# Performance work log

Measured on AMD Instinct MI355X. Metric: run time of the kernel, lower is better.

## Reference

```python
import jax, jax.numpy as jnp
import numpy as np

B, C, N = 16, 256, 2048  # C = channels_m, inputs have C//2 channels
C2 = C // 2
BN_EPS = 1e-5


def setup_inputs() -> dict:
    key = jax.random.key(0)
    ks = jax.random.split(key, 8)
    s = 1.0 / np.sqrt(C2)
    return {
        "q": jax.random.normal(ks[0], (B, C2, N), dtype=jnp.float32),
        "x": jax.random.normal(ks[1], (B, C2, N), dtype=jnp.float32),
        "Wq": jax.random.normal(ks[2], (C2, C2), dtype=jnp.float32) * s,
        "Wk": jax.random.normal(ks[3], (C2, C2), dtype=jnp.float32) * s,
        "Wv": jax.random.normal(ks[4], (C, C2), dtype=jnp.float32) * s,
        "bv": jax.random.normal(ks[5], (C,), dtype=jnp.float32) * 0.01,
        "Wt": jax.random.normal(ks[6], (C, C), dtype=jnp.float32) * (1.0 / np.sqrt(C)),
        "bt": jax.random.normal(ks[7], (C,), dtype=jnp.float32) * 0.01,
        "gamma": jnp.ones((C,), dtype=jnp.float32),
        "beta": jnp.zeros((C,), dtype=jnp.float32),
        "running_mean": jnp.zeros((C,), dtype=jnp.float32),
        "running_var": jnp.ones((C,), dtype=jnp.float32),
    }


def reference(q, x, Wq, Wk, Wv, bv, Wt, bt, gamma, beta, running_mean, running_var):
    # 1x1 Conv1d == channel matmul. q, x: [B, C2, N]
    x_q = jnp.einsum('oc,bcn->bno', Wq, q)                     # [B, N, C2]
    x_k = jnp.einsum('oc,bcn->bon', Wk, x)                     # [B, C2, N]
    x_v = jnp.einsum('oc,bcn->bon', Wv, q) + bv[None, :, None]  # [B, C, N]

    energy = jnp.einsum('bnc,bcm->bnm', x_q, x_k)              # [B, N, N]
    attn = jax.nn.softmax(energy, axis=-1)
    # extra column-wise L1 renormalization (offset-attention)
    attn = attn / (1e-9 + attn.sum(axis=1, keepdims=True))

    x_r = jnp.einsum('bcn,bnm->bcm', x_v, attn)                # [B, C, N]
    x2 = jnp.einsum('oc,bcn->bon', Wv, x) + bv[None, :, None]  # v_conv(x): [B, C, N]

    t = jnp.einsum('oc,bcn->bon', Wt, x2 - x_r) + bt[None, :, None]
    inv = gamma * jax.lax.rsqrt(running_var + BN_EPS)
    bn = t * inv[None, :, None] + (beta - running_mean * inv)[None, :, None]
    return jax.nn.relu(bn) + x2
```

## Files before the change

kernel.cpp:

```cpp
#include <hip/hip_runtime.h>
#include <hip/hip_bf16.h>
#include <math.h>

#define BB 16
#define CC 256
#define C2 128
#define NN 2048

typedef __attribute__((ext_vector_type(8))) _Float16 f16x8;
typedef __attribute__((ext_vector_type(8))) short bf16x8;
typedef __attribute__((ext_vector_type(16))) float f32x16;
typedef unsigned short u16;

#define OFF_X2   ((size_t)0)
#define OFF_U16  ((size_t)16777216)
#define UOFF_XQT ((size_t)0)
#define UOFF_XKT ((size_t)4194304)
#define UOFF_XV  ((size_t)8388608)
#define OFF_RMAX ((size_t)25165824)
#define OFF_RSUM ((size_t)25198592)
#define OFF_W16  ((size_t)29458432)
#define WOFF_WQ  ((size_t)0)
#define WOFF_WK  ((size_t)16384)
#define WOFF_WV  ((size_t)32768)
#define WOFF_WT  ((size_t)65536)

__device__ __forceinline__ u16 f2h(float f) {
    union { _Float16 h; u16 u; } v; v.h = (_Float16)f;
    return v.u;
}
__device__ __forceinline__ u16 f2bf(float f) {
    union { float f; unsigned u; } v; v.f = f;
    return (u16)((v.u + 0x7fffu + ((v.u >> 16) & 1u)) >> 16);
}

__global__ __launch_bounds__(256) void prep_w(
    const float* __restrict__ Wq, const float* __restrict__ Wk,
    const float* __restrict__ Wv, const float* __restrict__ Wt,
    u16* __restrict__ w16)
{
    int i = blockIdx.x * 256 + threadIdx.x;
    float v; u16* dst; int o, c, KC;
    if (i < 16384)      { v = Wq[i]; o = i >> 7; c = i & 127; KC = 16; dst = w16; }
    else if (i < 32768) { int j = i - 16384; v = Wk[j]; o = j >> 7; c = j & 127; KC = 16; dst = w16 + 16384; }
    else if (i < 65536) { int j = i - 32768; v = Wv[j]; o = j >> 7; c = j & 127; KC = 16; dst = w16 + 32768; }
    else                { int j = i - 65536; v = Wt[j]; o = j >> 8; c = j & 255; KC = 32; dst = w16 + 65536; }
    int idx = (((o >> 5) * KC + (c >> 3)) << 8) + ((o & 31) << 3) + (c & 7);
    dst[idx] = f2h(v);
}

__global__ __launch_bounds__(256, 2) void proj_fused(
    const float* __restrict__ q, const float* __restrict__ x,
    const u16* __restrict__ wq16, const u16* __restrict__ wk16,
    const u16* __restrict__ wv16, const float* __restrict__ bias,
    u16* __restrict__ xqT, u16* __restrict__ xkT,
    u16* __restrict__ xv_bf, float* __restrict__ x2_f32)
{
    __shared__ u16 t_s[64 * 136];
    __shared__ u16 st[16384];
    int tid = threadIdx.x, lane = tid & 63, wave = tid >> 6;
    int zb = blockIdx.z, b = zb >> 1, which = zb & 1;
    int n0 = blockIdx.x * 64;
    const float* in  = which ? x : q;
    const u16*   wqk = which ? wk16 : wq16;
    u16*         outT = which ? xkT : xqT;
    {
        int r = tid >> 2;
        int nc = (tid & 3) * 16;
        #pragma unroll
        for (int hh = 0; hh < 2; ++hh) {
            const float4* ip4 = (const float4*)(in + ((size_t)b * C2 + hh * 64 + r) * NN + n0 + nc);
            #pragma unroll
            for (int jj = 0; jj < 4; ++jj) {
                float4 v = ip4[jj];
                int nbase = nc + jj * 4;
                t_s[(nbase + 0) * 136 + hh * 64 + r] = f2h(v.x);
                t_s[(nbase + 1) * 136 + hh * 64 + r] = f2h(v.y);
                t_s[(nbase + 2) * 136 + hh * 64 + r] = f2h(v.z);
                t_s[(nbase + 3) * 136 + hh * 64 + r] = f2h(v.w);
            }
        }
    }
    __syncthreads();
    int nsub = wave & 1, g = wave >> 1;
    int lrow = lane & 31, h = lane >> 5, lk8 = h * 8;
    const u16* brow = &t_s[(nsub * 32 + lrow) * 136 + lk8];
    f32x16 aq0, aq1, av0, av1, av2, av3;
    #pragma unroll
    for (int r = 0; r < 16; ++r)
        { aq0[r]=0.f; aq1[r]=0.f; av0[r]=0.f; av1[r]=0.f; av2[r]=0.f; av3[r]=0.f; }
    const u16* wqA = wqk  + (size_t)(2 * g) * 4096 + h * 256 + lrow * 8;
    const u16* wvA = wv16 + (size_t)(4 * g) * 4096 + h * 256 + lrow * 8;
    #pragma unroll
    for (int kk = 0; kk < 8; ++kk) {
        f16x8 bf = *(const f16x8*)&brow[kk * 16];
        f16x8 q0 = *(const f16x8*)&wqA[kk * 512];
        f16x8 q1 = *(const f16x8*)&wqA[4096 + kk * 512];
        aq0 = __builtin_amdgcn_mfma_f32_32x32x16_f16(bf, q0, aq0, 0, 0, 0);
        aq1 = __builtin_amdgcn_mfma_f32_32x32x16_f16(bf, q1, aq1, 0, 0, 0);
        f16x8 v0 = *(const f16x8*)&wvA[kk * 512];
        f16x8 v1 = *(const f16x8*)&wvA[4096 + kk * 512];
        f16x8 v2 = *(const f16x8*)&wvA[8192 + kk * 512];
        f16x8 v3 = *(const f16x8*)&wvA[12288 + kk * 512];
        av0 = __builtin_amdgcn_mfma_f32_32x32x16_f16(v0, bf, av0, 0, 0, 0);
        av1 = __builtin_amdgcn_mfma_f32_32x32x16_f16(v1, bf, av1, 0, 0, 0);
        av2 = __builtin_amdgcn_mfma_f32_32x32x16_f16(v2, bf, av2, 0, 0, 0);
        av3 = __builtin_amdgcn_mfma_f32_32x32x16_f16(v3, bf, av3, 0, 0, 0);
    }
    __syncthreads();
    {
        int off = (nsub * 16 + g * 8 + (lrow >> 3)) * 256 + (lrow & 7);
        #pragma unroll
        for (int r = 0; r < 16; ++r) {
            int ro = (r & 3) + 8 * (r >> 2) + 4 * h;
            t_s[off + ro * 8]        = f2h(aq0[r]);
            t_s[off + 1024 + ro * 8] = f2h(aq1[r]);
        }
    }
    if (which == 0) {
        int off = (g * 4 * 8 + nsub * 4 + (lrow >> 3)) * 256 + (lrow & 7);
        #pragma unroll
        for (int r = 0; r < 16; ++r) {
            int ro = (r & 3) + 8 * (r >> 2) + 4 * h;
            int c0r = g * 128 + ro;
            st[off + ro * 8]        = f2bf(av0[r] + bias[c0r]);
            st[off + 2048 + ro * 8] = f2bf(av1[r] + bias[c0r + 32]);
            st[off + 4096 + ro * 8] = f2bf(av2[r] + bias[c0r + 64]);
            st[off + 6144 + ro * 8] = f2bf(av3[r] + bias[c0r + 96]);
        }
    }
    __syncthreads();
    {
        u16* outb = outT + (size_t)b * NN * C2 + (size_t)(n0 >> 5) * 4096;
        for (int i = tid; i < 1024; i += 256)
            *(uint4*)&outb[i * 8] = *(uint4*)&t_s[i * 8];
    }
    if (which == 0) {
        u16* xvb = xv_bf + (size_t)b * CC * NN + (size_t)(n0 >> 3) * 256;
        for (int i = tid; i < 2048; i += 256) {
            int ct = i >> 8, j = i & 255;
            *(uint4*)&xvb[(size_t)ct * 65536 + j * 8] = *(uint4*)&st[ct * 2048 + j * 8];
        }
    } else {
        int n = n0 + nsub * 32 + lrow;
        #pragma unroll
        for (int r = 0; r < 16; ++r) {
            int ro = (r & 3) + 8 * (r >> 2) + 4 * h;
            int c0r = g * 128 + ro;
            x2_f32[((size_t)b * CC + c0r) * NN + n]      = av0[r] + bias[c0r];
            x2_f32[((size_t)b * CC + c0r + 32) * NN + n] = av1[r] + bias[c0r + 32];
            x2_f32[((size_t)b * CC + c0r + 64) * NN + n] = av2[r] + bias[c0r + 64];
            x2_f32[((size_t)b * CC + c0r + 96) * NN + n] = av3[r] + bias[c0r + 96];
        }
    }
}

__global__ __launch_bounds__(512, 4) void rowstats_mfma(
    const u16* __restrict__ xqT, const u16* __restrict__ xkT,
    float* __restrict__ rmax, float* __restrict__ rsum)
{
    __shared__ float Mp[8][32];
    __shared__ float Sp[8][32];
    const int tid  = threadIdx.x;
    int flat = blockIdx.x + gridDim.x * blockIdx.y;
    int xcd = flat & 7, rank = flat >> 3;
    const int b  = xcd * 2 + (rank >> 5);
    const int n0 = (rank & 31) * 64;
    const int lane = tid & 63;
    const int wave = tid >> 6;
    const int lrow = lane & 31;
    const int h    = lane >> 5;
    const u16* xqb = xqT + (size_t)b * NN * C2;
    const u16* xkb = xkT + (size_t)b * NN * C2;
    const int mquad = wave >> 1, nsub = wave & 1;

    f16x8 bR[8];
    {
        const u16* bp = xqb + ((size_t)((n0 >> 5) + nsub) * 16) * 256 + h * 256 + lrow * 8;
        #pragma unroll
        for (int kk = 0; kk < 8; ++kk) bR[kk] = *(const f16x8*)&bp[kk * 512];
    }
    float runM = -1e30f, runS = 0.f;
    const u16* ap = xkb + (size_t)(mquad * 16) * 256 + h * 256 + lrow * 8;
    for (int m0 = 0; m0 < NN; m0 += 128) {
        f32x16 e0;
        #pragma unroll
        for (int r = 0; r < 16; ++r) e0[r] = 0.f;
        #pragma unroll
        for (int kk = 0; kk < 8; ++kk) {
            f16x8 a0 = *(const f16x8*)&ap[kk * 512];
            e0 = __builtin_amdgcn_mfma_f32_32x32x16_f16(a0, bR[kk], e0, 0, 0, 0);
        }
        ap += 16384;
        float tm = e0[0];
        #pragma unroll
        for (int r = 1; r < 16; ++r) tm = fmaxf(tm, e0[r]);
        float newM = fmaxf(runM, tm);
        float sc = __expf(runM - newM);
        float ts = 0.f;
        #pragma unroll
        for (int r = 0; r < 16; ++r) ts += __expf(e0[r] - newM);
        runS = runS * sc + ts;
        runM = newM;
    }
    float oM = __shfl_xor(runM, 32, 64);
    float oS = __shfl_xor(runS, 32, 64);
    float M2 = fmaxf(runM, oM);
    float S2 = runS * __expf(runM - M2) + oS * __expf(oM - M2);
    if (lane < 32) { Mp[wave][lane] = M2; Sp[wave][lane] = S2; }
    __syncthreads();
    if (tid < 64) {
        int ns = tid >> 5, li = tid & 31;
        float Ma = Mp[ns][li],     Mb = Mp[ns + 2][li];
        float Mc = Mp[ns + 4][li], Md = Mp[ns + 6][li];
        float Mf = fmaxf(fmaxf(Ma, Mb), fmaxf(Mc, Md));
        float Sf = Sp[ns][li]     * __expf(Ma - Mf) + Sp[ns + 2][li] * __expf(Mb - Mf)
                 + Sp[ns + 4][li] * __expf(Mc - Mf) + Sp[ns + 6][li] * __expf(Md - Mf);
        rmax[(size_t)b * NN + n0 + tid] = Mf;
        rsum[(size_t)b * NN + n0 + tid] = Sf;
    }
}

__global__ __launch_bounds__(512, 4) void pv_mfma(
    const u16* __restrict__ xqT, const u16* __restrict__ xkT,
    const u16* __restrict__ xv, const float* __restrict__ rmax,
    const float* __restrict__ rsum, const float* __restrict__ x2,
    const u16* __restrict__ wt16, const float* __restrict__ bt,
    const float* __restrict__ gamma, const float* __restrict__ beta,
    const float* __restrict__ rmean, const float* __restrict__ rvar,
    float* __restrict__ out)
{
    __shared__ __align__(16) u16 smem[19584];
    const int tid = threadIdx.x;
    int flat = blockIdx.x + gridDim.x * blockIdx.y;
    int xcd = flat & 7, rank = flat >> 3;
    const int b  = xcd * 2 + (rank >> 5);
    const int m0 = (rank & 31) * 64;
    const int lane = tid & 63;
    const int wave = tid >> 6;
    const int lrow = lane & 31;
    const int h    = lane >> 5;
    const int lk8  = h * 8;
    const u16* xqb = xqT + (size_t)b * NN * C2;
    const u16* xkb = xkT + (size_t)b * NN * C2;
    const u16* xvb = xv  + (size_t)b * CC * NN;
    const float* rmx = rmax + (size_t)b * NN;
    const float* rsm = rsum + (size_t)b * NN;

    if (tid < 256) {
        float iv = gamma[tid] * rsqrtf(rvar[tid] + 1e-5f);
        float* bn = (float*)(smem + 18560);
        bn[tid]       = iv;
        bn[256 + tid] = bt[tid] * iv + beta[tid] - rmean[tid] * iv;
    }

    f16x8 aK[8];
    {
        const u16* kp = xkb + ((size_t)((m0 >> 5) + (wave & 1)) * 16) * 256 + h * 256 + lrow * 8;
        #pragma unroll
        for (int kk = 0; kk < 8; ++kk) aK[kk] = *(const f16x8*)&kp[kk * 512];
    }
    const int nq = wave >> 1;
    const int nl = nq * 32 + lrow;
    const int mbase = (wave & 1) * 32 + 4 * h;
    const u16* bqbase = xqb + (size_t)nq * 4096 + h * 256 + lrow * 8;
    const u16* avbase = xvb + (size_t)wave * 65536 + h * 256 + lrow * 8;

    f32x16 acc00, acc01;
    #pragma unroll
    for (int r = 0; r < 16; ++r) { acc00[r] = 0.f; acc01[r] = 0.f; }
    float s_reg = 0.f;
    __syncthreads();

    for (int ph = 0; ph <= 16; ++ph) {
        f16x8 bq[8];
        float Mn = 0.f, Sn = 1.f;
        if (ph < 16) {
            const u16* bqp = bqbase + (size_t)ph * 16384;
            #pragma unroll
            for (int kk = 0; kk < 8; ++kk) bq[kk] = *(const f16x8*)&bqp[kk * 512];
            Mn = rmx[ph * 128 + nl];
            Sn = rsm[ph * 128 + nl];
        }
        if (ph >= 1) {
            const int t = ph - 1;
            const u16* p_prev = smem + (t & 1) * 8704;
            const u16* avp = avbase + (size_t)t * 4096;
            {
                const uint4* prp = (const uint4*)&p_prev[(tid & 63) * 136 + (tid >> 6) * 16];
                uint4 v0 = prp[0], v1 = prp[1];
                unsigned wsv[8] = {v0.x, v0.y, v0.z, v0.w, v1.x, v1.y, v1.z, v1.w};
                float ss = 0.f;
                #pragma unroll
                for (int j = 0; j < 8; ++j) {
                    union { unsigned u; float f; } lo, hi;
                    lo.u = wsv[j] << 16;
                    hi.u = wsv[j] & 0xffff0000u;
                    ss += lo.f + hi.f;
                }
                s_reg += ss;
            }
            const u16* br0 = &p_prev[lrow * 136 + lk8];
            const u16* br1 = &p_prev[(32 + lrow) * 136 + lk8];
            __builtin_amdgcn_s_setprio(1);
            #pragma unroll
            for (int kk = 0; kk < 8; ++kk) {
                bf16x8 a0 = *(const bf16x8*)&avp[kk * 512];
                bf16x8 b0 = *(const bf16x8*)&br0[kk * 16];
                bf16x8 b1 = *(const bf16x8*)&br1[kk * 16];
                acc00 = __builtin_amdgcn_mfma_f32_32x32x16_bf16(a0, b0, acc00, 0, 0, 0);
                acc01 = __builtin_amdgcn_mfma_f32_32x32x16_bf16(a0, b1, acc01, 0, 0, 0);
            }
            __builtin_amdgcn_s_setprio(0);
        }
        if (ph < 16) {
            f32x16 e0;
            #pragma unroll
            for (int r = 0; r < 16; ++r) e0[r] = 0.f;
            __builtin_amdgcn_s_setprio(1);
            #pragma unroll
            for (int kk = 0; kk < 8; ++kk)
                e0 = __builtin_amdgcn_mfma_f32_32x32x16_f16(aK[kk], bq[kk], e0, 0, 0, 0);
            __builtin_amdgcn_s_setprio(0);
            float Si = 1.f / Sn;
            u16* p_cur = smem + (ph & 1) * 8704;
            #pragma unroll
            for (int r = 0; r < 16; ++r) {
                int ml = mbase + (r & 3) + 8 * (r >> 2);
                p_cur[ml * 136 + nl] = f2bf(__expf(e0[r] - Mn) * Si);
            }
        }
        __syncthreads();
    }
    float* s_part = (float*)(smem + 17408);
    s_part[(tid & 63) * 8 + (tid >> 6)] = s_reg;
    __syncthreads();
    float* sinv = (float*)(smem + 18432);
    if (tid < 64) {
        float ss = 0.f;
        #pragma unroll
        for (int j = 0; j < 8; ++j) ss += s_part[tid * 8 + j];
        sinv[tid] = 1.f / (1e-9f + ss);
    }
    __syncthreads();
    u16* dts = smem;
    const float* x2b = x2 + (size_t)b * CC * NN;
    float si0 = sinv[lrow], si1 = sinv[32 + lrow];
    #pragma unroll
    for (int r = 0; r < 16; ++r) {
        int ro = (r & 3) + 8 * (r >> 2) + 4 * h;
        int c = wave * 32 + ro;
        float d0 = x2b[(size_t)c * NN + m0 + lrow]      - acc00[r] * si0;
        float d1 = x2b[(size_t)c * NN + m0 + 32 + lrow] - acc01[r] * si1;
        dts[lrow * 264 + c]        = f2h(d0);
        dts[(32 + lrow) * 264 + c] = f2h(d1);
    }
    __syncthreads();
    {
        float* inv_s = (float*)(smem + 18560);
        float* add_s = inv_s + 256;
        int rt0 = (wave >> 1) * 2;
        int ns2 = wave & 1;
        const u16* brow2 = &dts[(ns2 * 32 + lrow) * 264 + lk8];
        const u16* a0p = wt16 + (size_t)rt0 * 8192 + h * 256 + lrow * 8;
        const u16* a1p = a0p + 8192;
        f32x16 o0a, o1a;
        #pragma unroll
        for (int r = 0; r < 16; ++r) { o0a[r] = 0.f; o1a[r] = 0.f; }
        #pragma unroll
        for (int kk = 0; kk < 16; ++kk) {
            f16x8 bb2 = *(const f16x8*)&brow2[kk * 16];
            f16x8 a0 = *(const f16x8*)&a0p[kk * 512];
            f16x8 a1 = *(const f16x8*)&a1p[kk * 512];
            o0a = __builtin_amdgcn_mfma_f32_32x32x16_f16(a0, bb2, o0a, 0, 0, 0);
            o1a = __builtin_amdgcn_mfma_f32_32x32x16_f16(a1, bb2, o1a, 0, 0, 0);
        }
        int n = m0 + ns2 * 32 + lrow;
        float* outb = out + (size_t)b * CC * NN;
        #pragma unroll
        for (int r = 0; r < 16; ++r) {
            int ro = (r & 3) + 8 * (r >> 2) + 4 * h;
            int ol0 = rt0 * 32 + ro, ol1 = ol0 + 32;
            float t0 = o0a[r] * inv_s[ol0] + add_s[ol0];
            float t1 = o1a[r] * inv_s[ol1] + add_s[ol1];
            outb[(size_t)ol0 * NN + n] = fmaxf(t0, 0.f) + x2b[(size_t)ol0 * NN + n];
            outb[(size_t)ol1 * NN + n] = fmaxf(t1, 0.f) + x2b[(size_t)ol1 * NN + n];
        }
    }
}

extern "C" void kernel_launch(void* const* d_in, const int* in_sizes, int n_in,
                              void* d_out, int out_size, void* d_ws, size_t ws_size,
                              hipStream_t stream)
{
    const float* q     = (const float*)d_in[0];
    const float* x     = (const float*)d_in[1];
    const float* Wq    = (const float*)d_in[2];
    const float* Wk    = (const float*)d_in[3];
    const float* Wv    = (const float*)d_in[4];
    const float* bv    = (const float*)d_in[5];
    const float* Wt    = (const float*)d_in[6];
    const float* bt    = (const float*)d_in[7];
    const float* gamma = (const float*)d_in[8];
    const float* beta  = (const float*)d_in[9];
    const float* rmean = (const float*)d_in[10];
    const float* rvar  = (const float*)d_in[11];
    float* out = (float*)d_out;
    float* ws  = (float*)d_ws;

    float* x2   = ws + OFF_X2;
    u16*   u1   = (u16*)(ws + OFF_U16);
    u16*   xqT  = u1 + UOFF_XQT;
    u16*   xkT  = u1 + UOFF_XKT;
    u16*   xv   = u1 + UOFF_XV;
    float* rmax = ws + OFF_RMAX;
    float* rsum = ws + OFF_RSUM;
    u16*   w16  = (u16*)(ws + OFF_W16);

    dim3 blk(256);
    prep_w<<<dim3(512), blk, 0, stream>>>(Wq, Wk, Wv, Wt, w16);
    proj_fused<<<dim3(NN/64, 1, 2*BB), blk, 0, stream>>>(
        q, x, w16 + WOFF_WQ, w16 + WOFF_WK, w16 + WOFF_WV, bv,
        xqT, xkT, xv, x2);
    rowstats_mfma<<<dim3(NN/64, BB), dim3(512), 0, stream>>>(xqT, xkT, rmax, rsum);
    pv_mfma<<<dim3(NN/64, BB), dim3(512), 0, stream>>>(
        xqT, xkT, xv, rmax, rsum, x2, w16 + WOFF_WT, bt, gamma, beta,
        rmean, rvar, out);
}
```

Measured before the change: 249.7 us.

## Merge all stages into one cooperative persistent kernel with grid syncs

Replaces the four separate launches (weight prep, projection, row stats, PV+output) with one cooperative kernel. The stages are separated by grid.sync, and each block loops over work units in a grid-stride loop. The projection stage is reorganised for 512-thread blocks: each block handles both the q and x inputs for one tile, so per-wave accumulator usage is lower. The aim is to remove launch gaps and inter-kernel drain, at the cost of grid-barrier overhead and occupancy limited by the cooperative launch.

```diff
diff --git a/kernel.cpp b/kernel.cpp
--- a/kernel.cpp
+++ b/kernel.cpp
@@ -1,6 +1,9 @@
 #include <hip/hip_runtime.h>
+#include <hip/hip_cooperative_groups.h>
 #include <hip/hip_bf16.h>
 #include <math.h>
+
+namespace cg = cooperative_groups;
 
 #define BB 16
 #define CC 256
@@ -34,357 +37,362 @@
     return (u16)((v.u + 0x7fffu + ((v.u >> 16) & 1u)) >> 16);
 }
 
-__global__ __launch_bounds__(256) void prep_w(
+__global__ __launch_bounds__(512, 4) void fused_all(
+    const float* __restrict__ q, const float* __restrict__ x,
     const float* __restrict__ Wq, const float* __restrict__ Wk,
-    const float* __restrict__ Wv, const float* __restrict__ Wt,
-    u16* __restrict__ w16)
+    const float* __restrict__ Wv, const float* __restrict__ bv,
+    const float* __restrict__ Wt, const float* __restrict__ bt,
+    const float* __restrict__ gamma, const float* __restrict__ beta,
+    const float* __restrict__ rmean, const float* __restrict__ rvar,
+    float* __restrict__ out, float* __restrict__ ws)
 {
-    int i = blockIdx.x * 256 + threadIdx.x;
-    float v; u16* dst; int o, c, KC;
-    if (i < 16384)      { v = Wq[i]; o = i >> 7; c = i & 127; KC = 16; dst = w16; }
-    else if (i < 32768) { int j = i - 16384; v = Wk[j]; o = j >> 7; c = j & 127; KC = 16; dst = w16 + 16384; }
-    else if (i < 65536) { int j = i - 32768; v = Wv[j]; o = j >> 7; c = j & 127; KC = 16; dst = w16 + 32768; }
-    else                { int j = i - 65536; v = Wt[j]; o = j >> 8; c = j & 255; KC = 32; dst = w16 + 65536; }
-    int idx = (((o >> 5) * KC + (c >> 3)) << 8) + ((o & 31) << 3) + (c & 7);
-    dst[idx] = f2h(v);
-}
-
-__global__ __launch_bounds__(256, 2) void proj_fused(
-    const float* __restrict__ q, const float* __restrict__ x,
-    const u16* __restrict__ wq16, const u16* __restrict__ wk16,
-    const u16* __restrict__ wv16, const float* __restrict__ bias,
-    u16* __restrict__ xqT, u16* __restrict__ xkT,
-    u16* __restrict__ xv_bf, float* __restrict__ x2_f32)
-{
-    __shared__ u16 t_s[64 * 136];
-    __shared__ u16 st[16384];
-    int tid = threadIdx.x, lane = tid & 63, wave = tid >> 6;
-    int zb = blockIdx.z, b = zb >> 1, which = zb & 1;
-    int n0 = blockIdx.x * 64;
-    const float* in  = which ? x : q;
-    const u16*   wqk = which ? wk16 : wq16;
-    u16*         outT = which ? xkT : xqT;
-    {
-        int r = tid >> 2;
-        int nc = (tid & 3) * 16;
+    float* x2   = ws + OFF_X2;
+    u16*   u1   = (u16*)(ws + OFF_U16);
+    u16*   xqT  = u1 + UOFF_XQT;
+    u16*   xkT  = u1 + UOFF_XKT;
+    u16*   xv   = u1 + UOFF_XV;
+    float* rmax = ws + OFF_RMAX;
+    float* rsum = ws + OFF_RSUM;
+    u16*   w16  = (u16*)(ws + OFF_W16);
+
+    __shared__ __align__(16) u16 smem[19584];
+    const int tid = threadIdx.x;
+    const int nb  = gridDim.x;
+    cg::grid_group grid = cg::this_grid();
+
+    for (int i = blockIdx.x * 512 + tid; i < 131072; i += nb * 512) {
+        float v; u16* dst; int o, c, KC;
+        if (i < 16384)      { v = Wq[i]; o = i >> 7; c = i & 127; KC = 16; dst = w16; }
+        else if (i < 32768) { int j = i - 16384; v = Wk[j]; o = j >> 7; c = j & 127; KC = 16; dst = w16 + 16384; }
+        else if (i < 65536) { int j = i - 32768; v = Wv[j]; o = j >> 7; c = j & 127; KC = 16; dst = w16 + 32768; }
+        else                { int j = i - 65536; v = Wt[j]; o = j >> 8; c = j & 255; KC = 32; dst = w16 + 65536; }
+        dst[(((o >> 5) * KC + (c >> 3)) << 8) + ((o & 31) << 3) + (c & 7)] = f2h(v);
+    }
+    __threadfence();
+    grid.sync();
+
+    for (int wu = blockIdx.x; wu < 512; wu += nb) {
+        const int lane = tid & 63, wave = tid >> 6;
+        const int lrow = lane & 31, h = lane >> 5, lk8 = h * 8;
+        const int b  = wu & 15;
+        const int n0 = (wu >> 4) * 64;
+        const int nsub = wave & 1, gp = wave >> 1;
+        u16* t_s = smem;
+        u16* stg = smem + 8704;
+        const u16* wv16 = w16 + WOFF_WV;
+
         #pragma unroll
-        for (int hh = 0; hh < 2; ++hh) {
-            const float4* ip4 = (const float4*)(in + ((size_t)b * C2 + hh * 64 + r) * NN + n0 + nc);
-            #pragma unroll
-            for (int jj = 0; jj < 4; ++jj) {
-                float4 v = ip4[jj];
-                int nbase = nc + jj * 4;
-                t_s[(nbase + 0) * 136 + hh * 64 + r] = f2h(v.x);
-                t_s[(nbase + 1) * 136 + hh * 64 + r] = f2h(v.y);
-                t_s[(nbase + 2) * 136 + hh * 64 + r] = f2h(v.z);
-                t_s[(nbase + 3) * 136 + hh * 64 + r] = f2h(v.w);
+        for (int u = 0; u < 2; ++u) {
+            const float* in  = u ? x : q;
+            const u16*   wqk = u ? (w16 + WOFF_WK) : (w16 + WOFF_WQ);
+            __syncthreads();
+            {
+                int c = tid >> 2;
+                int qn = (tid & 3) * 16;
+                const float4* ip4 = (const float4*)(in + ((size_t)b * C2 + c) * NN + n0 + qn);
+                #pragma unroll
+                for (int jj = 0; jj < 4; ++jj) {
+                    float4 v = ip4[jj];
+                    int nbv = qn + jj * 4;
+                    t_s[(nbv + 0) * 136 + c] = f2h(v.x);
+                    t_s[(nbv + 1) * 136 + c] = f2h(v.y);
+                    t_s[(nbv + 2) * 136 + c] = f2h(v.z);
+                    t_s[(nbv + 3) * 136 + c] = f2h(v.w);
+                }
+            }
+            __syncthreads();
+            f32x16 aq0, av0, av1;
+            #pragma unroll
+            for (int r = 0; r < 16; ++r) { aq0[r] = 0.f; av0[r] = 0.f; av1[r] = 0.f; }
+            const u16* brow = &t_s[(nsub * 32 + lrow) * 136 + lk8];
+            const u16* wqA  = wqk  + (size_t)gp * 4096 + h * 256 + lrow * 8;
+            const u16* wvA0 = wv16 + (size_t)(gp * 2) * 4096 + h * 256 + lrow * 8;
+            const u16* wvA1 = wvA0 + 4096;
+            #pragma unroll
+            for (int kk = 0; kk < 8; ++kk) {
+                f16x8 bf = *(const f16x8*)&brow[kk * 16];
+                f16x8 q0 = *(const f16x8*)&wqA[kk * 512];
+                aq0 = __builtin_amdgcn_mfma_f32_32x32x16_f16(bf, q0, aq0, 0, 0, 0);
+                f16x8 v0 = *(const f16x8*)&wvA0[kk * 512];
+                f16x8 v1 = *(const f16x8*)&wvA1[kk * 512];
+                av0 = __builtin_amdgcn_mfma_f32_32x32x16_f16(v0, bf, av0, 0, 0, 0);
+                av1 = __builtin_amdgcn_mfma_f32_32x32x16_f16(v1, bf, av1, 0, 0, 0);
+            }
+            {
+                int off = (nsub * 16 + gp * 4 + (lrow >> 3)) * 256 + (lrow & 7);
+                #pragma unroll
+                for (int r = 0; r < 16; ++r) {
+                    int ro = (r & 3) + 8 * (r >> 2) + 4 * h;
+                    stg[off + ro * 8] = f2h(aq0[r]);
+                }
+            }
+            __syncthreads();
+            {
+                u16* outb = (u ? xkT : xqT) + (size_t)b * NN * C2 + (size_t)(n0 >> 5) * 4096;
+                for (int i = tid; i < 1024; i += 512)
+                    *(uint4*)&outb[i * 8] = *(uint4*)&stg[i * 8];
+            }
+            if (u == 0) {
+                #pragma unroll
+                for (int ct2 = 0; ct2 < 2; ++ct2) {
+                    __syncthreads();
+                    if ((gp >> 1) == ct2) {
+                        int off = (((gp & 1) * 2) * 8 + nsub * 4 + (lrow >> 3)) * 256 + (lrow & 7);
+                        #pragma unroll
+                        for (int r = 0; r < 16; ++r) {
+                            int ro = (r & 3) + 8 * (r >> 2) + 4 * h;
+                            int c0 = gp * 64 + ro;
+                            stg[off + ro * 8]        = f2bf(av0[r] + bv[c0]);
+                            stg[off + 2048 + ro * 8] = f2bf(av1[r] + bv[c0 + 32]);
+                        }
+                    }
+                    __syncthreads();
+                    u16* xvb = xv + (size_t)b * CC * NN + (size_t)(ct2 * 4) * 65536
+                                  + (size_t)(n0 >> 3) * 256;
+                    for (int i = tid; i < 1024; i += 512) {
+                        int ctile = i >> 8;
+                        int m8 = (i & 255) * 8;
+                        *(uint4*)&xvb[(size_t)ctile * 65536 + m8] =
+                            *(uint4*)&stg[ctile * 2048 + m8];
+                    }
+                }
+            } else {
+                float* x2b = x2 + (size_t)b * CC * NN;
+                int n = n0 + nsub * 32 + lrow;
+                #pragma unroll
+                for (int r = 0; r < 16; ++r) {
+                    int ro = (r & 3) + 8 * (r >> 2) + 4 * h;
+                    int c0 = gp * 64 + ro;
+                    x2b[(size_t)c0 * NN + n]        = av0[r] + bv[c0];
+                    x2b[(size_t)(c0 + 32) * NN + n] = av1[r] + bv[c0 + 32];
+                }
             }
         }
     }
-    __syncthreads();
-    int nsub = wave & 1, g = wave >> 1;
-    int lrow = lane & 31, h = lane >> 5, lk8 = h * 8;
-    const u16* brow = &t_s[(nsub * 32 + lrow) * 136 + lk8];
-    f32x16 aq0, aq1, av0, av1, av2, av3;
-    #pragma unroll
-    for (int r = 0; r < 16; ++r)
-        { aq0[r]=0.f; aq1[r]=0.f; av0[r]=0.f; av1[r]=0.f; av2[r]=0.f; av3[r]=0.f; }
-    const u16* wqA = wqk  + (size_t)(2 * g) * 4096 + h * 256 + lrow * 8;
-    const u16* wvA = wv16 + (size_t)(4 * g) * 4096 + h * 256 + lrow * 8;
-    #pragma unroll
-    for (int kk = 0; kk < 8; ++kk) {
-        f16x8 bf = *(const f16x8*)&brow[kk * 16];
-        f16x8 q0 = *(const f16x8*)&wqA[kk * 512];
-        f16x8 q1 = *(const f16x8*)&wqA[4096 + kk * 512];
-        aq0 = __builtin_amdgcn_mfma_f32_32x32x16_f16(bf, q0, aq0, 0, 0, 0);
-        aq1 = __builtin_amdgcn_mfma_f32_32x32x16_f16(bf, q1, aq1, 0, 0, 0);
-        f16x8 v0 = *(const f16x8*)&wvA[kk * 512];
-        f16x8 v1 = *(const f16x8*)&wvA[4096 + kk * 512];
-        f16x8 v2 = *(const f16x8*)&wvA[8192 + kk * 512];
-        f16x8 v3 = *(const f16x8*)&wvA[12288 + kk * 512];
-        av0 = __builtin_amdgcn_mfma_f32_32x32x16_f16(v0, bf, av0, 0, 0, 0);
-        av1 = __builtin_amdgcn_mfma_f32_32x32x16_f16(v1, bf, av1, 0, 0, 0);
-        av2 = __builtin_amdgcn_mfma_f32_32x32x16_f16(v2, bf, av2, 0, 0, 0);
-        av3 = __builtin_amdgcn_mfma_f32_32x32x16_f16(v3, bf, av3, 0, 0, 0);
+    __threadfence();
+    grid.sync();
+
+    for (int wu = blockIdx.x; wu < 512; wu += nb) {
+        __syncthreads();
+        float* Mp = (float*)smem;
+        float* Sp = Mp + 256;
+        const int lane = tid & 63;
+        const int wave = tid >> 6;
+        const int lrow = lane & 31;
+        const int h    = lane >> 5;
+        int xcd = wu & 7, rank = wu >> 3;
+        const int b  = xcd * 2 + (rank >> 5);
+        const int n0 = (rank & 31) * 64;
+        const u16* xqb = xqT + (size_t)b * NN * C2;
+        const u16* xkb = xkT + (size_t)b * NN * C2;
+        const int mquad = wave >> 1, nsub = wave & 1;
+
+        f16x8 bR[8];
+        {
+            const u16* bp = xqb + ((size_t)((n0 >> 5) + nsub) * 16) * 256 + h * 256 + lrow * 8;
+            #pragma unroll
+            for (int kk = 0; kk < 8; ++kk) bR[kk] = *(const f16x8*)&bp[kk * 512];
+        }
+        float runM = -1e30f, runS = 0.f;
+        const u16* ap = xkb + (size_t)(mquad * 16) * 256 + h * 256 + lrow * 8;
+        for (int m0 = 0; m0 < NN; m0 += 128) {
+            f32x16 e0;
+            #pragma unroll
+            for (int r = 0; r < 16; ++r) e0[r] = 0.f;
+            #pragma unroll
+            for (int kk = 0; kk < 8; ++kk) {
+                f16x8 a0 = *(const f16x8*)&ap[kk * 512];
+                e0 = __builtin_amdgcn_mfma_f32_32x32x16_f16(a0, bR[kk], e0, 0, 0, 0);
+            }
+            ap += 16384;
+            float tm = e0[0];
+            #pragma unroll
+            for (int r = 1; r < 16; ++r) tm = fmaxf(tm, e0[r]);
+            float newM = fmaxf(runM, tm);
+            float sc = __expf(runM - newM);
+            float ts = 0.f;
+            #pragma unroll
+            for (int r = 0; r < 16; ++r) ts += __expf(e0[r] - newM);
+            runS = runS * sc + ts;
+            runM = newM;
+        }
+        float oM = __shfl_xor(runM, 32, 64);
+        float oS = __shfl_xor(runS, 32, 64);
+        float M2 = fmaxf(runM, oM);
+        float S2 = runS * __expf(runM - M2) + oS * __expf(oM - M2);
+        if (lane < 32) { Mp[wave * 32 + lane] = M2; Sp[wave * 32 + lane] = S2; }
+        __syncthreads();
+        if (tid < 64) {
+            int ns = tid >> 5, li = tid & 31;
+            float Ma = Mp[ns * 32 + li],       Mb = Mp[(ns + 2) * 32 + li];
+            float Mc = Mp[(ns + 4) * 32 + li], Md = Mp[(ns + 6) * 32 + li];
+            float Mf = fmaxf(fmaxf(Ma, Mb), fmaxf(Mc, Md));
+            float Sf = Sp[ns * 32 + li]       * __expf(Ma - Mf)
+                     + Sp[(ns + 2) * 32 + li] * __expf(Mb - Mf)
+                     + Sp[(ns + 4) * 32 + li] * __expf(Mc - Mf)
+                     + Sp[(ns + 6) * 32 + li] * __expf(Md - Mf);
+            rmax[(size_t)b * NN + n0 + tid] = Mf;
+            rsum[(size_t)b * NN + n0 + tid] = Sf;
+        }
     }
-    __syncthreads();
-    {
-        int off = (nsub * 16 + g * 8 + (lrow >> 3)) * 256 + (lrow & 7);
+    __threadfence();
+    grid.sync();
+
+    for (int wu = blockIdx.x; wu < 512; wu += nb) {
+        __syncthreads();
+        const int lane = tid & 63;
+        const int wave = tid >> 6;
+        const int lrow = lane & 31;
+        const int h    = lane >> 5;
+        const int lk8  = h * 8;
+        int xcd = wu & 7, rank = wu >> 3;
+        const int b  = xcd * 2 + (rank >> 5);
+        const int m0 = (rank & 31) * 64;
+        const u16* xqb = xqT + (size_t)b * NN * C2;
+        const u16* xkb = xkT + (size_t)b * NN * C2;
+        const u16* xvb = xv  + (size_t)b * CC * NN;
+        const float* rmx = rmax + (size_t)b * NN;
+        const float* rsm = rsum + (size_t)b * NN;
+        const u16* wt16 = w16 + WOFF_WT;
+
+        if (tid < 256) {
+            float iv = gamma[tid] * rsqrtf(rvar[tid] + 1e-5f);
+            float* bn = (float*)(smem + 18560);
+            bn[tid]       = iv;
+            bn[256 + tid] = bt[tid] * iv + beta[tid] - rmean[tid] * iv;
+        }
+        f16x8 aK[8];
+        {
+            const u16* kp = xkb + ((size_t)((m0 >> 5) + (wave & 1)) * 16) * 256 + h * 256 + lrow * 8;
+            #pragma unroll
+            for (int kk = 0; kk < 8; ++kk) aK[kk] = *(const f16x8*)&kp[kk * 512];
+        }
+        const int nq = wave >> 1;
+        const int nl = nq * 32 + lrow;
+        const int mbase = (wave & 1) * 32 + 4 * h;
+        const u16* bqbase = xqb + (size_t)nq * 4096 + h * 256 + lrow * 8;
+        const u16* avbase = xvb + (size_t)wave * 65536 + h * 256 + lrow * 8;
+
+        f32x16 acc00, acc01;
+        #pragma unroll
+        for (int r = 0; r < 16; ++r) { acc00[r] = 0.f; acc01[r] = 0.f; }
+        float s_reg = 0.f;
+        __syncthreads();
+
+        for (int ph = 0; ph <= 16; ++ph) {
+            f16x8 bq[8];
+            float Mn = 0.f, Sn = 1.f;
+            if (ph < 16) {
+                const u16* bqp = bqbase + (size_t)ph * 16384;
+                #pragma unroll
+                for (int kk = 0; kk < 8; ++kk) bq[kk] = *(const f16x8*)&bqp[kk * 512];
+                Mn = rmx[ph * 128 + nl];
+                Sn = rsm[ph * 128 + nl];
+            }
+            if (ph >= 1) {
+                const int t = ph - 1;
+                const u16* p_prev = smem + (t & 1) * 8704;
+                const u16* avp = avbase + (size_t)t * 4096;
+                {
+                    const uint4* prp = (const uint4*)&p_prev[(tid & 63) * 136 + (tid >> 6) * 16];
+                    uint4 v0 = prp[0], v1 = prp[1];
+                    unsigned wsv[8] = {v0.x, v0.y, v0.z, v0.w, v1.x, v1.y, v1.z, v1.w};
+                    float ss = 0.f;
+                    #pragma unroll
+                    for (int j = 0; j < 8; ++j) {
+                        union { unsigned u; float f; } lo, hi;
+                        lo.u = wsv[j] << 16;
+                        hi.u = wsv[j] & 0xffff0000u;
+                        ss += lo.f + hi.f;
+                    }
+                    s_reg += ss;
+                }
+                const u16* br0 = &p_prev[lrow * 136 + lk8];
+                const u16* br1 = &p_prev[(32 + lrow) * 136 + lk8];
+                __builtin_amdgcn_s_setprio(1);
+                #pragma unroll
+                for (int kk = 0; kk < 8; ++kk) {
+                    bf16x8 a0 = *(const bf16x8*)&avp[kk * 512];
+                    bf16x8 b0 = *(const bf16x8*)&br0[kk * 16];
+                    bf16x8 b1 = *(const bf16x8*)&br1[kk * 16];
+                    acc00 = __builtin_amdgcn_mfma_f32_32x32x16_bf16(a0, b0, acc00, 0, 0, 0);
+                    acc01 = __builtin_amdgcn_mfma_f32_32x32x16_bf16(a0, b1, acc01, 0, 0, 0);
+                }
+                __builtin_amdgcn_s_setprio(0);
+            }
+            if (ph < 16) {
+                f32x16 e0;
+                #pragma unroll
+                for (int r = 0; r < 16; ++r) e0[r] = 0.f;
+                __builtin_amdgcn_s_setprio(1);
+                #pragma unroll
+                for (int kk = 0; kk < 8; ++kk)
+                    e0 = __builtin_amdgcn_mfma_f32_32x32x16_f16(aK[kk], bq[kk], e0, 0, 0, 0);
+                __builtin_amdgcn_s_setprio(0);
+                float Si = 1.f / Sn;
+                u16* p_cur = smem + (ph & 1) * 8704;
+                #pragma unroll
+                for (int r = 0; r < 16; ++r) {
+                    int ml = mbase + (r & 3) + 8 * (r >> 2);
+                    p_cur[ml * 136 + nl] = f2bf(__expf(e0[r] - Mn) * Si);
+                }
+            }
+            __syncthreads();
+        }
+        float* s_part = (float*)(smem + 17408);
+        s_part[(tid & 63) * 8 + (tid >> 6)] = s_reg;
+        __syncthreads();
+        float* sinv = (float*)(smem + 18432);
+        if (tid < 64) {
+            float ss = 0.f;
+            #pragma unroll
+            for (int j = 0; j < 8; ++j) ss += s_part[tid * 8 + j];
+            sinv[tid] = 1.f / (1e-9f + ss);
+        }
+        __syncthreads();
+        u16* dts = smem;
+        const float* x2b = x2 + (size_t)b * CC * NN;
+        float si0 = sinv[lrow], si1 = sinv[32 + lrow];
         #pragma unroll
         for (int r = 0; r < 16; ++r) {
             int ro = (r & 3) + 8 * (r >> 2) + 4 * h;
-            t_s[off + ro * 8]        = f2h(aq0[r]);
-            t_s[off + 1024 + ro * 8] = f2h(aq1[r]);
-        }
-    }
-    if (which == 0) {
-        int off = (g * 4 * 8 + nsub * 4 + (lrow >> 3)) * 256 + (lrow & 7);
-        #pragma unroll
-        for (int r = 0; r < 16; ++r) {
-            int ro = (r & 3) + 8 * (r >> 2) + 4 * h;
-            int c0r = g * 128 + ro;
-            st[off + ro * 8]        = f2bf(av0[r] + bias[c0r]);
-            st[off + 2048 + ro * 8] = f2bf(av1[r] + bias[c0r + 32]);
-            st[off + 4096 + ro * 8] = f2bf(av2[r] + bias[c0r + 64]);
-            st[off + 6144 + ro * 8] = f2bf(av3[r] + bias[c0r + 96]);
-        }
-    }
-    __syncthreads();
-    {
-        u16* outb = outT + (size_t)b * NN * C2 + (size_t)(n0 >> 5) * 4096;
-        for (int i = tid; i < 1024; i += 256)
-            *(uint4*)&outb[i * 8] = *(uint4*)&t_s[i * 8];
-    }
-    if (which == 0) {
-        u16* xvb = xv_bf + (size_t)b * CC * NN + (size_t)(n0 >> 3) * 256;
-        for (int i = tid; i < 2048; i += 256) {
-            int ct = i >> 8, j = i & 255;
-            *(uint4*)&xvb[(size_t)ct * 65536 + j * 8] = *(uint4*)&st[ct * 2048 + j * 8];
-        }
-    } else {
-        int n = n0 + nsub * 32 + lrow;
-        #pragma unroll
-        for (int r = 0; r < 16; ++r) {
-            int ro = (r & 3) + 8 * (r >> 2) + 4 * h;
-            int c0r = g * 128 + ro;
-            x2_f32[((size_t)b * CC + c0r) * NN + n]      = av0[r] + bias[c0r];
-            x2_f32[((size_t)b * CC + c0r + 32) * NN + n] = av1[r] + bias[c0r + 32];
-            x2_f32[((size_t)b * CC + c0r + 64) * NN + n] = av2[r] + bias[c0r + 64];
-            x2_f32[((size_t)b * CC + c0r + 96) * NN + n] = av3[r] + bias[c0r + 96];
-        }
-    }
-}
-
-__global__ __launch_bounds__(512, 4) void rowstats_mfma(
-    const u16* __restrict__ xqT, const u16* __restrict__ xkT,
-    float* __restrict__ rmax, float* __restrict__ rsum)
-{
-    __shared__ float Mp[8][32];
-    __shared__ float Sp[8][32];
-    const int tid  = threadIdx.x;
-    int flat = blockIdx.x + gridDim.x * blockIdx.y;
-    int xcd = flat & 7, rank = flat >> 3;
-    const int b  = xcd * 2 + (rank >> 5);
-    const int n0 = (rank & 31) * 64;
-    const int lane = tid & 63;
-    const int wave = tid >> 6;
-    const int lrow = lane & 31;
-    const int h    = lane >> 5;
-    const u16* xqb = xqT + (size_t)b * NN * C2;
-    const u16* xkb = xkT + (size_t)b * NN * C2;
-    const int mquad = wave >> 1, nsub = wave & 1;
-
-    f16x8 bR[8];
-    {
-        const u16* bp = xqb + ((size_t)((n0 >> 5) + nsub) * 16) * 256 + h * 256 + lrow * 8;
-        #pragma unroll
-        for (int kk = 0; kk < 8; ++kk) bR[kk] = *(const f16x8*)&bp[kk * 512];
-    }
-    float runM = -1e30f, runS = 0.f;
-    const u16* ap = xkb + (size_t)(mquad * 16) * 256 + h * 256 + lrow * 8;
-    for (int m0 = 0; m0 < NN; m0 += 128) {
-        f32x16 e0;
-        #pragma unroll
-        for (int r = 0; r < 16; ++r) e0[r] = 0.f;
-        #pragma unroll
-        for (int kk = 0; kk < 8; ++kk) {
-            f16x8 a0 = *(const f16x8*)&ap[kk * 512];
-            e0 = __builtin_amdgcn_mfma_f32_32x32x16_f16(a0, bR[kk], e0, 0, 0, 0);
-        }
-        ap += 16384;
-        float tm = e0[0];
-        #pragma unroll
-        for (int r = 1; r < 16; ++r) tm = fmaxf(tm, e0[r]);
-        float newM = fmaxf(runM, tm);
-        float sc = __expf(runM - newM);
-        float ts = 0.f;
-        #pragma unroll
-        for (int r = 0; r < 16; ++r) ts += __expf(e0[r] - newM);
-        runS = runS * sc + ts;
-        runM = newM;
-    }
-    float oM = __shfl_xor(runM, 32, 64);
-    float oS = __shfl_xor(runS, 32, 64);
-    float M2 = fmaxf(runM, oM);
-    float S2 = runS * __expf(runM - M2) + oS * __expf(oM - M2);
-    if (lane < 32) { Mp[wave][lane] = M2; Sp[wave][lane] = S2; }
-    __syncthreads();
-    if (tid < 64) {
-        int ns = tid >> 5, li = tid & 31;
-        float Ma = Mp[ns][li],     Mb = Mp[ns + 2][li];
-        float Mc = Mp[ns + 4][li], Md = Mp[ns + 6][li];
-        float Mf = fmaxf(fmaxf(Ma, Mb), fmaxf(Mc, Md));
-        float Sf = Sp[ns][li]     * __expf(Ma - Mf) + Sp[ns + 2][li] * __expf(Mb - Mf)
-                 + Sp[ns + 4][li] * __expf(Mc - Mf) + Sp[ns + 6][li] * __expf(Md - Mf);
-        rmax[(size_t)b * NN + n0 + tid] = Mf;
-        rsum[(size_t)b * NN + n0 + tid] = Sf;
-    }
-}
-
-__global__ __launch_bounds__(512, 4) void pv_mfma(
-    const u16* __restrict__ xqT, const u16* __restrict__ xkT,
-    const u16* __restrict__ xv, const float* __restrict__ rmax,
-    const float* __restrict__ rsum, const float* __restrict__ x2,
-    const u16* __restrict__ wt16, const float* __restrict__ bt,
-    const float* __restrict__ gamma, const float* __restrict__ beta,
-    const float* __restrict__ rmean, const float* __restrict__ rvar,
-    float* __restrict__ out)
-{
-    __shared__ __align__(16) u16 smem[19584];
-    const int tid = threadIdx.x;
-    int flat = blockIdx.x + gridDim.x * blockIdx.y;
-    int xcd = flat & 7, rank = flat >> 3;
-    const int b  = xcd * 2 + (rank >> 5);
-    const int m0 = (rank & 31) * 64;
-    const int lane = tid & 63;
-    const int wave = tid >> 6;
-    const int lrow = lane & 31;
-    const int h    = lane >> 5;
-    const int lk8  = h * 8;
-    const u16* xqb = xqT + (size_t)b * NN * C2;
-    const u16* xkb = xkT + (size_t)b * NN * C2;
-    const u16* xvb = xv  + (size_t)b * CC * NN;
-    const float* rmx = rmax + (size_t)b * NN;
-    const float* rsm = rsum + (size_t)b * NN;
-
-    if (tid < 256) {
-        float iv = gamma[tid] * rsqrtf(rvar[tid] + 1e-5f);
-        float* bn = (float*)(smem + 18560);
-        bn[tid]       = iv;
-        bn[256 + tid] = bt[tid] * iv + beta[tid] - rmean[tid] * iv;
-    }
-
-    f16x8 aK[8];
-    {
-        const u16* kp = xkb + ((size_t)((m0 >> 5) + (wave & 1)) * 16) * 256 + h * 256 + lrow * 8;
-        #pragma unroll
-        for (int kk = 0; kk < 8; ++kk) aK[kk] = *(const f16x8*)&kp[kk * 512];
-    }
-    const int nq = wave >> 1;
-    const int nl = nq * 32 + lrow;
-    const int mbase = (wave & 1) * 32 + 4 * h;
-    const u16* bqbase = xqb + (size_t)nq * 4096 + h * 256 + lrow * 8;
-    const u16* avbase = xvb + (size_t)wave * 65536 + h * 256 + lrow * 8;
-
-    f32x16 acc00, acc01;
-    #pragma unroll
-    for (int r = 0; r < 16; ++r) { acc00[r] = 0.f; acc01[r] = 0.f; }
-    float s_reg = 0.f;
-    __syncthreads();
-
-    for (int ph = 0; ph <= 16; ++ph) {
-        f16x8 bq[8];
-        float Mn = 0.f, Sn = 1.f;
-        if (ph < 16) {
-            const u16* bqp = bqbase + (size_t)ph * 16384;
-            #pragma unroll
-            for (int kk = 0; kk < 8; ++kk) bq[kk] = *(const f16x8*)&bqp[kk * 512];
-            Mn = rmx[ph * 128 + nl];
-            Sn = rsm[ph * 128 + nl];
-        }
-        if (ph >= 1) {
-            const int t = ph - 1;
-            const u16* p_prev = smem + (t & 1) * 8704;
-            const u16* avp = avbase + (size_t)t * 4096;
-            {
-                const uint4* prp = (const uint4*)&p_prev[(tid & 63) * 136 + (tid >> 6) * 16];
-                uint4 v0 = prp[0], v1 = prp[1];
-                unsigned wsv[8] = {v0.x, v0.y, v0.z, v0.w, v1.x, v1.y, v1.z, v1.w};
-                float ss = 0.f;
-                #pragma unroll
-                for (int j = 0; j < 8; ++j) {
-                    union { unsigned u; float f; } lo, hi;
-                    lo.u = wsv[j] << 16;
-                    hi.u = wsv[j] & 0xffff0000u;
-                    ss += lo.f + hi.f;
-                }
-                s_reg += ss;
-            }
-            const u16* br0 = &p_prev[lrow * 136 + lk8];
-            const u16* br1 = &p_prev[(32 + lrow) * 136 + lk8];
-            __builtin_amdgcn_s_setprio(1);
-            #pragma unroll
-            for (int kk = 0; kk < 8; ++kk) {
-                bf16x8 a0 = *(const bf16x8*)&avp[kk * 512];
-                bf16x8 b0 = *(const bf16x8*)&br0[kk * 16];
-                bf16x8 b1 = *(const bf16x8*)&br1[kk * 16];
-                acc00 = __builtin_amdgcn_mfma_f32_32x32x16_bf16(a0, b0, acc00, 0, 0, 0);
-                acc01 = __builtin_amdgcn_mfma_f32_32x32x16_bf16(a0, b1, acc01, 0, 0, 0);
-            }
-            __builtin_amdgcn_s_setprio(0);
-        }
-        if (ph < 16) {
-            f32x16 e0;
-            #pragma unroll
-            for (int r = 0; r < 16; ++r) e0[r] = 0.f;
-            __builtin_amdgcn_s_setprio(1);
-            #pragma unroll
-            for (int kk = 0; kk < 8; ++kk)
-                e0 = __builtin_amdgcn_mfma_f32_32x32x16_f16(aK[kk], bq[kk], e0, 0, 0, 0);
-            __builtin_amdgcn_s_setprio(0);
-            float Si = 1.f / Sn;
-            u16* p_cur = smem + (ph & 1) * 8704;
+            int c = wave * 32 + ro;
+            float d0 = x2b[(size_t)c * NN + m0 + lrow]      - acc00[r] * si0;
+            float d1 = x2b[(size_t)c * NN + m0 + 32 + lrow] - acc01[r] * si1;
+            dts[lrow * 264 + c]        = f2h(d0);
+            dts[(32 + lrow) * 264 + c] = f2h(d1);
+        }
+        __syncthreads();
+        {
+            float* inv_s = (float*)(smem + 18560);
+            float* add_s = inv_s + 256;
+            int rt0 = (wave >> 1) * 2;
+            int ns2 = wave & 1;
+            const u16* brow2 = &dts[(ns2 * 32 + lrow) * 264 + lk8];
+            const u16* a0p = wt16 + (size_t)rt0 * 8192 + h * 256 + lrow * 8;
+            const u16* a1p = a0p + 8192;
+            f32x16 o0a, o1a;
+            #pragma unroll
+            for (int r = 0; r < 16; ++r) { o0a[r] = 0.f; o1a[r] = 0.f; }
+            #pragma unroll
+            for (int kk = 0; kk < 16; ++kk) {
+                f16x8 bb2 = *(const f16x8*)&brow2[kk * 16];
+                f16x8 a0 = *(const f16x8*)&a0p[kk * 512];
+                f16x8 a1 = *(const f16x8*)&a1p[kk * 512];
+                o0a = __builtin_amdgcn_mfma_f32_32x32x16_f16(a0, bb2, o0a, 0, 0, 0);
+                o1a = __builtin_amdgcn_mfma_f32_32x32x16_f16(a1, bb2, o1a, 0, 0, 0);
+            }
+            int n = m0 + ns2 * 32 + lrow;
+            float* outb = out + (size_t)b * CC * NN;
             #pragma unroll
             for (int r = 0; r < 16; ++r) {
-                int ml = mbase + (r & 3) + 8 * (r >> 2);
-                p_cur[ml * 136 + nl] = f2bf(__expf(e0[r] - Mn) * Si);
-            }
-        }
-        __syncthreads();
-    }
-    float* s_part = (float*)(smem + 17408);
-    s_part[(tid & 63) * 8 + (tid >> 6)] = s_reg;
-    __syncthreads();
-    float* sinv = (float*)(smem + 18432);
-    if (tid < 64) {
-        float ss = 0.f;
-        #pragma unroll
-        for (int j = 0; j < 8; ++j) ss += s_part[tid * 8 + j];
-        sinv[tid] = 1.f / (1e-9f + ss);
-    }
-    __syncthreads();
-    u16* dts = smem;
-    const float* x2b = x2 + (size_t)b * CC * NN;
-    float si0 = sinv[lrow], si1 = sinv[32 + lrow];
-    #pragma unroll
-    for (int r = 0; r < 16; ++r) {
-        int ro = (r & 3) + 8 * (r >> 2) + 4 * h;
-        int c = wave * 32 + ro;
-        float d0 = x2b[(size_t)c * NN + m0 + lrow]      - acc00[r] * si0;
-        float d1 = x2b[(size_t)c * NN + m0 + 32 + lrow] - acc01[r] * si1;
-        dts[lrow * 264 + c]        = f2h(d0);
-        dts[(32 + lrow) * 264 + c] = f2h(d1);
-    }
-    __syncthreads();
-    {
-        float* inv_s = (float*)(smem + 18560);
-        float* add_s = inv_s + 256;
-        int rt0 = (wave >> 1) * 2;
-        int ns2 = wave & 1;
-        const u16* brow2 = &dts[(ns2 * 32 + lrow) * 264 + lk8];
-        const u16* a0p = wt16 + (size_t)rt0 * 8192 + h * 256 + lrow * 8;
-        const u16* a1p = a0p + 8192;
-        f32x16 o0a, o1a;
-        #pragma unroll
-        for (int r = 0; r < 16; ++r) { o0a[r] = 0.f; o1a[r] = 0.f; }
-        #pragma unroll
-        for (int kk = 0; kk < 16; ++kk) {
-            f16x8 bb2 = *(const f16x8*)&brow2[kk * 16];
-            f16x8 a0 = *(const f16x8*)&a0p[kk * 512];
-            f16x8 a1 = *(const f16x8*)&a1p[kk * 512];
-            o0a = __builtin_amdgcn_mfma_f32_32x32x16_f16(a0, bb2, o0a, 0, 0, 0);
-            o1a = __builtin_amdgcn_mfma_f32_32x32x16_f16(a1, bb2, o1a, 0, 0, 0);
-        }
-        int n = m0 + ns2 * 32 + lrow;
-        float* outb = out + (size_t)b * CC * NN;
-        #pragma unroll
-        for (int r = 0; r < 16; ++r) {
-            int ro = (r & 3) + 8 * (r >> 2) + 4 * h;
-            int ol0 = rt0 * 32 + ro, ol1 = ol0 + 32;
-            float t0 = o0a[r] * inv_s[ol0] + add_s[ol0];
-            float t1 = o1a[r] * inv_s[ol1] + add_s[ol1];
-            outb[(size_t)ol0 * NN + n] = fmaxf(t0, 0.f) + x2b[(size_t)ol0 * NN + n];
-            outb[(size_t)ol1 * NN + n] = fmaxf(t1, 0.f) + x2b[(size_t)ol1 * NN + n];
+                int ro = (r & 3) + 8 * (r >> 2) + 4 * h;
+                int ol0 = rt0 * 32 + ro, ol1 = ol0 + 32;
+                float t0 = o0a[r] * inv_s[ol0] + add_s[ol0];
+                float t1 = o1a[r] * inv_s[ol1] + add_s[ol1];
+                outb[(size_t)ol0 * NN + n] = fmaxf(t0, 0.f) + x2b[(size_t)ol0 * NN + n];
+                outb[(size_t)ol1 * NN + n] = fmaxf(t1, 0.f) + x2b[(size_t)ol1 * NN + n];
+            }
         }
     }
 }
@@ -408,22 +416,27 @@
     float* out = (float*)d_out;
     float* ws  = (float*)d_ws;
 
-    float* x2   = ws + OFF_X2;
-    u16*   u1   = (u16*)(ws + OFF_U16);
-    u16*   xqT  = u1 + UOFF_XQT;
-    u16*   xkT  = u1 + UOFF_XKT;
-    u16*   xv   = u1 + UOFF_XV;
-    float* rmax = ws + OFF_RMAX;
-    float* rsum = ws + OFF_RSUM;
-    u16*   w16  = (u16*)(ws + OFF_W16);
-
-    dim3 blk(256);
-    prep_w<<<dim3(512), blk, 0, stream>>>(Wq, Wk, Wv, Wt, w16);
-    proj_fused<<<dim3(NN/64, 1, 2*BB), blk, 0, stream>>>(
-        q, x, w16 + WOFF_WQ, w16 + WOFF_WK, w16 + WOFF_WV, bv,
-        xqT, xkT, xv, x2);
-    rowstats_mfma<<<dim3(NN/64, BB), dim3(512), 0, stream>>>(xqT, xkT, rmax, rsum);
-    pv_mfma<<<dim3(NN/64, BB), dim3(512), 0, stream>>>(
-        xqT, xkT, xv, rmax, rsum, x2, w16 + WOFF_WT, bt, gamma, beta,
-        rmean, rvar, out);
+    static int nblocks = 0;
+    if (nblocks == 0) {
+        int maxb = 0;
+        if (hipOccupancyMaxActiveBlocksPerMultiprocessor(
+                &maxb, (const void*)fused_all, 512, 0) != hipSuccess || maxb < 1)
+            maxb = 1;
+        int dev = 0, ncu = 0;
+        hipGetDevice(&dev);
+        if (hipDeviceGetAttribute(&ncu, hipDeviceAttributeMultiprocessorCount,
+                                  dev) != hipSuccess || ncu < 1)
+            ncu = 256;
+        long cap = (long)maxb * (long)ncu;
+        nblocks = (int)(cap < 512 ? cap : 512);
+        if (nblocks < 1) nblocks = 256;
+    }
+
+    void* args[] = {
+        (void*)&q, (void*)&x, (void*)&Wq, (void*)&Wk, (void*)&Wv, (void*)&bv,
+        (void*)&Wt, (void*)&bt, (void*)&gamma, (void*)&beta, (void*)&rmean,
+        (void*)&rvar, (void*)&out, (void*)&ws
+    };
+    hipLaunchCooperativeKernel((const void*)fused_all, dim3(nblocks), dim3(512),
+                               args, 0, stream);
 }
```

Result: slower. 656.9 us (+163.1%).
